# Kernel tuning notes

Hardware: AMD Instinct MI355X
Metric: run time of the kernel (lower is better)

The kernel has to match this reference:

```python
import jax, jax.numpy as jnp
import numpy as np

HEADS = 16
DIM_HEAD = 64
LN_EPS = 1e-5


def setup_inputs() -> dict:
    key = jax.random.key(0)
    ks = jax.random.split(key, 4)
    b, n, dim = 2, 2048, 1024
    inner = HEADS * DIM_HEAD
    x = jax.random.normal(ks[0], (b, n, dim), dtype=jnp.float32)
    gamma = jnp.ones((dim,), dtype=jnp.float32)
    beta = jnp.zeros((dim,), dtype=jnp.float32)
    w_qkv = jax.random.normal(ks[1], (dim, 3 * inner), dtype=jnp.float32) * (dim ** -0.5)
    w_out = jax.random.normal(ks[2], (inner, dim), dtype=jnp.float32) * (inner ** -0.5)
    b_out = jnp.zeros((dim,), dtype=jnp.float32)
    return {"x": x, "gamma": gamma, "beta": beta, "w_qkv": w_qkv, "w_out": w_out, "b_out": b_out}


def reference(x, gamma, beta, w_qkv, w_out, b_out):
    b, n, dim = x.shape
    h, d = HEADS, DIM_HEAD
    scale = d ** -0.5
    # LayerNorm
    mu = jnp.mean(x, axis=-1, keepdims=True)
    var = jnp.mean(jnp.square(x - mu), axis=-1, keepdims=True)
    xn = (x - mu) * jax.lax.rsqrt(var + LN_EPS) * gamma + beta
    # QKV projection (no bias)
    qkv = xn @ w_qkv  # [b, n, 3*h*d]
    q, k, v = jnp.split(qkv, 3, axis=-1)
    split_heads = lambda t: t.reshape(b, n, h, d).transpose(0, 2, 1, 3)  # [b, h, n, d]
    q, k, v = split_heads(q), split_heads(k), split_heads(v)
    q = q * scale
    sim = jnp.einsum('bhid,bhjd->bhij', q, k)  # full O(n^2) score matrix
    attn = jax.nn.softmax(sim, axis=-1)
    out = jnp.einsum('bhij,bhjd->bhid', attn, v)
    out = out.transpose(0, 2, 1, 3).reshape(b, n, h * d)
    return out @ w_out + b_out
```

## Files before the change

kernel.cpp:

```cpp
#include <hip/hip_runtime.h>
#include <hip/hip_bf16.h>

#define HEADS 16
#define DH 64
#define DIM 1024
#define SEQ 2048
#define BATCH 2
#define ROWS (BATCH*SEQ)
#define NQKV (3*DIM)
#define NKVT (SEQ/64)
#define NSPLIT 2
#define QSCALE 0.18033688011112042f
#define NBH (BATCH*HEADS)
#define NQROWS (NBH*SEQ)

typedef __attribute__((ext_vector_type(8))) short bf16x8;
typedef __attribute__((ext_vector_type(4))) float f32x4;
typedef __attribute__((ext_vector_type(16))) float f32x16;
typedef __attribute__((ext_vector_type(4))) unsigned u32x4;
typedef __hip_bfloat16 bf16;

static __device__ __forceinline__ bf16 f2bf(float v){ return __float2bfloat16(v); }

static __device__ __forceinline__ unsigned cvtpk(float a, float b){
  unsigned r;
  asm("v_cvt_pk_bf16_f32 %0, %1, %2" : "=v"(r) : "v"(a), "v"(b));
  return r;
}

static __device__ __forceinline__ void gload16(const void* g, void* lds){
  __builtin_amdgcn_global_load_lds((const __attribute__((address_space(1))) void*)g,
                                   (__attribute__((address_space(3))) void*)lds, 16, 0, 0);
}

__global__ __launch_bounds__(256) void prep_kernel(
    const float* __restrict__ x, const float* __restrict__ gamma,
    const float* __restrict__ beta, bf16* __restrict__ xn,
    const float* __restrict__ w_qkv, bf16* __restrict__ wqt,
    const float* __restrict__ w_out, bf16* __restrict__ wot)
{
  __shared__ float red[8];
  __shared__ __align__(16) bf16 tt[64][72];
  int bid = blockIdx.x;
  int tid = threadIdx.x;
  if (bid < ROWS){
    int row = bid;
    float4 v = ((const float4*)(x + (size_t)row*DIM))[tid];
    float s  = v.x+v.y+v.z+v.w;
    float ss = v.x*v.x+v.y*v.y+v.z*v.z+v.w*v.w;
    #pragma unroll
    for (int m=1;m<64;m<<=1){ s += __shfl_xor(s,m); ss += __shfl_xor(ss,m); }
    int wid = tid>>6;
    if ((tid&63)==0){ red[wid]=s; red[4+wid]=ss; }
    __syncthreads();
    s  = red[0]+red[1]+red[2]+red[3];
    ss = red[4]+red[5]+red[6]+red[7];
    float mu  = s*(1.0f/DIM);
    float var = ss*(1.0f/DIM) - mu*mu;
    float inv = rsqrtf(var + 1e-5f);
    float4 g  = ((const float4*)gamma)[tid];
    float4 bb = ((const float4*)beta)[tid];
    __align__(8) bf16 o[4];
    o[0]=f2bf((v.x-mu)*inv*g.x+bb.x);
    o[1]=f2bf((v.y-mu)*inv*g.y+bb.y);
    o[2]=f2bf((v.z-mu)*inv*g.z+bb.z);
    o[3]=f2bf((v.w-mu)*inv*g.w+bb.w);
    *(uint2*)&xn[(size_t)row*DIM + tid*4] = *(const uint2*)o;
    return;
  }
  const float* in; bf16* out; int R, C, bx, by;
  if (bid < ROWS + 768){
    int idx = bid - ROWS; bx = idx % 48; by = idx / 48;
    in = w_qkv; out = wqt; R = DIM; C = NQKV;
  } else {
    int idx = bid - ROWS - 768; bx = idx % 16; by = idx / 16;
    in = w_out; out = wot; R = DIM; C = DIM;
  }
  int c0 = bx*64, r0 = by*64;
  int row = tid>>2;
  int cq  = (tid&3)*16;
  #pragma unroll
  for (int j=0;j<4;j++){
    float4 v = *(const float4*)&in[(size_t)(r0+row)*C + c0 + cq + j*4];
    tt[cq+j*4+0][row] = f2bf(v.x);
    tt[cq+j*4+1][row] = f2bf(v.y);
    tt[cq+j*4+2][row] = f2bf(v.z);
    tt[cq+j*4+3][row] = f2bf(v.w);
  }
  __syncthreads();
  int c = tid>>2; int rq = (tid&3)*16;
  uint4 u0 = *(const uint4*)&tt[c][rq];
  uint4 u1 = *(const uint4*)&tt[c][rq+8];
  *(uint4*)&out[(size_t)(c0+c)*R + r0 + rq]     = u0;
  *(uint4*)&out[(size_t)(c0+c)*R + r0 + rq + 8] = u1;
}

template<int BM>
__global__ __launch_bounds__(256) void gemm_bt(
    const bf16* __restrict__ A, const bf16* __restrict__ Bt, int K, int mode,
    bf16* __restrict__ qb, bf16* __restrict__ kb, bf16* __restrict__ vtb,
    float* __restrict__ outf, const float* __restrict__ bias)
{
  constexpr int MT = (BM == 128) ? 4 : 2;
  constexpr int NT = (BM == 128) ? 4 : 2;
  __shared__ __align__(16) bf16 aL[3][BM*32];
  __shared__ __align__(16) bf16 bL[3][BM*32];
  int tid = threadIdx.x;
  int w = tid>>6, l = tid&63;
  int lr = l&15, lh = l>>4;
  int wr = w>>1, wc = w&1;
  int nbx = gridDim.x;
  int lin = blockIdx.y*nbx + blockIdx.x;
  int cpx = (nbx*gridDim.y) >> 3;
  int nl  = (lin & 7)*cpx + (lin >> 3);
  int bx = nl % nbx, by = nl / nbx;
  const bf16* Ab = A  + (size_t)(by*BM)*K;
  const bf16* Bb = Bt + (size_t)(bx*BM)*K;
  int srow = w*32 + (l>>2);
  int scol = ((l&3)*8) ^ (((l>>2)&3)<<3);
  int frsw = (lr&3)<<3;
  int nt = K/32;

  f32x4 acc[MT][NT] = {};

  auto STAGE = [&](int buf, int k0){
    if constexpr (BM == 128){
      gload16(Ab + (size_t)(srow   )*K + k0 + scol, &aL[buf][w*1024      ]);
      gload16(Ab + (size_t)(srow+16)*K + k0 + scol, &aL[buf][w*1024 + 512]);
      gload16(Bb + (size_t)(srow   )*K + k0 + scol, &bL[buf][w*1024      ]);
      gload16(Bb + (size_t)(srow+16)*K + k0 + scol, &bL[buf][w*1024 + 512]);
    } else {
      gload16(Ab + (size_t)(tid>>2)*K + k0 + scol, &aL[buf][w*512]);
      gload16(Bb + (size_t)(tid>>2)*K + k0 + scol, &bL[buf][w*512]);
    }
  };

  auto COMPUTE = [&](int buf){
    bf16x8 af[MT], bfr[NT];
    #pragma unroll
    for (int m=0;m<MT;m++)
      af[m]  = *(const bf16x8*)&aL[buf][(wr*(MT*16) + m*16 + lr)*32 + ((lh*8) ^ frsw)];
    #pragma unroll
    for (int n=0;n<NT;n++)
      bfr[n] = *(const bf16x8*)&bL[buf][(wc*(NT*16) + n*16 + lr)*32 + ((lh*8) ^ frsw)];
    #pragma unroll
    for (int m=0;m<MT;m++)
      #pragma unroll
      for (int n=0;n<NT;n++)
        acc[m][n] = __builtin_amdgcn_mfma_f32_16x16x32_bf16(af[m], bfr[n], acc[m][n], 0,0,0);
  };

  STAGE(0, 0);
  STAGE(1, 32);
  int cur = 0;
  for (int t=0; t<nt-1; t++){
    if constexpr (BM == 128) asm volatile("s_waitcnt vmcnt(4)" ::: "memory");
    else                     asm volatile("s_waitcnt vmcnt(2)" ::: "memory");
    __builtin_amdgcn_s_barrier();
    __builtin_amdgcn_sched_barrier(0);
    int s2 = cur + 2; if (s2 >= 3) s2 -= 3;
    if (t+2 < nt) STAGE(s2, (t+2)*32);
    COMPUTE(cur);
    cur = (cur == 2) ? 0 : cur + 1;
  }
  asm volatile("s_waitcnt vmcnt(0)" ::: "memory");
  __builtin_amdgcn_s_barrier();
  __builtin_amdgcn_sched_barrier(0);
  COMPUTE(cur);

  int rb = by*BM + wr*(MT*16), cb = bx*BM + wc*(NT*16);
  if (mode == 1){
    #pragma unroll
    for (int m=0;m<MT;m++)
      #pragma unroll
      for (int n=0;n<NT;n++)
        #pragma unroll
        for (int reg=0;reg<4;reg++){
          int r = rb + m*16 + lh*4 + reg;
          int c = cb + n*16 + lr;
          outf[(size_t)r*DIM + c] = acc[m][n][reg] + bias[c];
        }
  } else if (bx < 8){
    int b = rb >> 11;
    int nn0 = rb & 2047;
    #pragma unroll
    for (int m=0;m<MT;m++)
      #pragma unroll
      for (int n=0;n<NT;n++)
        #pragma unroll
        for (int reg=0;reg<4;reg++){
          int nn = nn0 + m*16 + lh*4 + reg;
          int c  = cb + n*16 + lr;
          int hh = c >> 6, dd = c & 63;
          qb[((size_t)(b*HEADS + hh)*SEQ + nn)*DH + dd] = f2bf(acc[m][n][reg]*QSCALE);
        }
  } else if (bx < 16){
    int b = rb >> 11;
    int kvt = (rb & 2047) >> 6;
    int hh0 = ((cb - 1024) >> 6);
    #pragma unroll
    for (int m=0;m<MT;m++)
      #pragma unroll
      for (int reg=0;reg<4;reg++){
        int kvi = m*16 + lh*4 + reg;
        int sw  = (kvi&7)<<3;
        #pragma unroll
        for (int n=0;n<NT;n++){
          int dd = n*16 + lr;
          kb[((size_t)(b*HEADS + hh0)*NKVT + kvt)*4096 + kvi*64 + (dd ^ sw)] = f2bf(acc[m][n][reg]);
        }
      }
  } else {
    __syncthreads();
    bf16* tl = (w < 2 ? (bf16*)aL : (bf16*)bL) + (w&1)*4096;
    int b   = rb >> 11;
    int kvt = (rb & 2047) >> 6;
    int hh  = (cb - 2048) >> 6;
    #pragma unroll
    for (int n=0;n<NT;n++){
      int dd = n*16 + lr;
      int sw = (dd&7)<<3;
      #pragma unroll
      for (int m=0;m<MT;m++)
        #pragma unroll
        for (int reg=0;reg<4;reg++)
          tl[dd*64 + ((m*16 + lh*4 + reg) ^ sw)] = f2bf(acc[m][n][reg]);
    }
    __syncthreads();
    size_t gb = ((size_t)(b*HEADS + hh)*NKVT + kvt)*4096;
    #pragma unroll
    for (int j=0;j<8;j++)
      *(uint4*)&vtb[gb + j*512 + l*8] = *(const uint4*)&tl[j*512 + l*8];
  }
}

__global__ __launch_bounds__(256,4) void attn_part(
    const bf16* __restrict__ qb, const bf16* __restrict__ kb,
    const bf16* __restrict__ vtb,
    bf16* __restrict__ Opart, float* __restrict__ Mpart, float* __restrict__ Spart)
{
  __shared__ __align__(16) bf16 Kl[2][4096];
  __shared__ __align__(16) bf16 Vl[2][4096];
  int tid = threadIdx.x;
  int w = tid>>6, l = tid&63;
  int q5 = l & 31;
  int hi = l >> 5;
  int swz = (q5&7)<<3;
  int lin = (blockIdx.z*gridDim.y + blockIdx.y)*gridDim.x + blockIdx.x;
  int nl  = (lin & 7)*128 + (lin >> 3);
  int bqx = nl & 15;
  int bh  = (nl >> 4) & 31;
  int sp  = nl >> 9;
  int ts = sp*16, te = ts+16;
  const bf16* Q  = qb  + (size_t)bh*SEQ*DH;
  const bf16* Kt = kb  + (size_t)bh*NKVT*4096;
  const bf16* Vt = vtb + (size_t)bh*NKVT*4096;
  int q0w = bqx*128 + w*32;

  int co[4];
  #pragma unroll
  for (int st=0;st<4;st++) co[st] = (st*16 + hi*8) ^ swz;
  int r0 = q5*64, r1 = r0 + 2048;

  bf16x8 qf[4];
  #pragma unroll
  for (int st=0;st<4;st++)
    qf[st] = *(const bf16x8*)&Q[(size_t)(q0w + q5)*DH + st*16 + hi*8];

  bf16x8 vone;
  #pragma unroll
  for (int i=0;i<8;i++) vone[i] = (short)0x3f80;

  f32x16 o0 = {}, o1 = {}, osum = {};
  float mrun = -3e38f;

  {
    const bf16* ks = Kt + (size_t)ts*4096;
    const bf16* vs = Vt + (size_t)ts*4096;
    gload16(ks + w*1024       + l*8, &Kl[0][w*1024      ]);
    gload16(ks + w*1024 + 512 + l*8, &Kl[0][w*1024 + 512]);
    gload16(vs + w*1024       + l*8, &Vl[0][w*1024      ]);
    gload16(vs + w*1024 + 512 + l*8, &Vl[0][w*1024 + 512]);
  }

  for (int t=ts; t<te; t++){
    int cur = (t-ts)&1;
    __syncthreads();
    if (t+1 < te){
      const bf16* ks = Kt + (size_t)(t+1)*4096;
      const bf16* vs = Vt + (size_t)(t+1)*4096;
      gload16(ks + w*1024       + l*8, &Kl[cur^1][w*1024      ]);
      gload16(ks + w*1024 + 512 + l*8, &Kl[cur^1][w*1024 + 512]);
      gload16(vs + w*1024       + l*8, &Vl[cur^1][w*1024      ]);
      gload16(vs + w*1024 + 512 + l*8, &Vl[cur^1][w*1024 + 512]);
    }
    f32x16 s0 = {}, s1 = {};
    __builtin_amdgcn_s_setprio(1);
    #pragma unroll
    for (int st=0;st<4;st++){
      bf16x8 kf0 = *(const bf16x8*)&Kl[cur][r0 + co[st]];
      bf16x8 kf1 = *(const bf16x8*)&Kl[cur][r1 + co[st]];
      s0 = __builtin_amdgcn_mfma_f32_32x32x16_bf16(kf0, qf[st], s0, 0,0,0);
      s1 = __builtin_amdgcn_mfma_f32_32x32x16_bf16(kf1, qf[st], s1, 0,0,0);
    }
    __builtin_amdgcn_s_setprio(0);
    float pm = -3e38f;
    #pragma unroll
    for (int r=0;r<16;r++) pm = fmaxf(fmaxf(pm, s0[r]), s1[r]);
    pm = fmaxf(pm, __shfl_xor(pm, 32));
    if (__any(pm > mrun + 8.f)){
      float mn = fmaxf(mrun, pm);
      float sc = __builtin_amdgcn_exp2f(mrun - mn);
      mrun = mn;
      #pragma unroll
      for (int reg=0;reg<16;reg++){
        float scr = __shfl(sc, (l & 32) | ((reg&3) + 8*(reg>>2) + 4*hi));
        o0[reg] *= scr;
        o1[reg] *= scr;
        osum[reg] *= scr;
      }
    }
    #pragma unroll
    for (int r=0;r<16;r++){
      s0[r] = __builtin_amdgcn_exp2f(s0[r] - mrun);
      s1[r] = __builtin_amdgcn_exp2f(s1[r] - mrun);
    }
    #define PV_STEP(SV, SGN, KVS)                                                    \
    {                                                                                \
      unsigned Aw = cvtpk(SV[SGN+0], SV[SGN+1]);                                     \
      unsigned Bw = cvtpk(SV[SGN+2], SV[SGN+3]);                                     \
      unsigned Cw = cvtpk(SV[SGN+4], SV[SGN+5]);                                     \
      unsigned Dw = cvtpk(SV[SGN+6], SV[SGN+7]);                                     \
      asm volatile("v_permlane32_swap_b32 %0, %1" : "+v"(Aw), "+v"(Cw));             \
      asm volatile("v_permlane32_swap_b32 %0, %1" : "+v"(Bw), "+v"(Dw));             \
      u32x4 pw = {Aw, Bw, Cw, Dw};                                                   \
      bf16x8 pa = *(const bf16x8*)&pw;                                               \
      bf16x8 vf0 = *(const bf16x8*)&Vl[cur][r0 + co[KVS]];                           \
      bf16x8 vf1 = *(const bf16x8*)&Vl[cur][r1 + co[KVS]];                           \
      __builtin_amdgcn_s_setprio(1);                                                 \
      o0 = __builtin_amdgcn_mfma_f32_32x32x16_bf16(pa, vf0, o0, 0,0,0);              \
      o1 = __builtin_amdgcn_mfma_f32_32x32x16_bf16(pa, vf1, o1, 0,0,0);              \
      osum = __builtin_amdgcn_mfma_f32_32x32x16_bf16(pa, vone, osum, 0,0,0);         \
      __builtin_amdgcn_s_setprio(0);                                                 \
    }
    PV_STEP(s0, 0, 0)
    PV_STEP(s0, 8, 1)
    PV_STEP(s1, 0, 2)
    PV_STEP(s1, 8, 3)
    #undef PV_STEP
  }
  size_t rbase = ((size_t)sp*NBH + bh)*SEQ;
  #pragma unroll
  for (int reg=0;reg<16;reg++){
    int q = q0w + (reg&3) + 8*(reg>>2) + 4*hi;
    Opart[(rbase + q)*64 + q5]      = f2bf(o0[reg]);
    Opart[(rbase + q)*64 + 32 + q5] = f2bf(o1[reg]);
  }
  if (l < 32)
    Mpart[rbase + q0w + l] = mrun;
  if (q5 == 0){
    #pragma unroll
    for (int reg=0;reg<16;reg++){
      int q = q0w + (reg&3) + 8*(reg>>2) + 4*hi;
      Spart[rbase + q] = osum[reg];
    }
  }
}

__global__ __launch_bounds__(256) void attn_merge(
    const bf16* __restrict__ Opart, const float* __restrict__ Mpart,
    const float* __restrict__ Spart, bf16* __restrict__ ao)
{
  int r = blockIdx.x*4 + (threadIdx.x>>6);
  int d = threadIdx.x & 63;
  float m0 = Mpart[r], m1 = Mpart[NQROWS + r];
  float m  = fmaxf(m0, m1);
  float c0 = exp2f(m0 - m), c1 = exp2f(m1 - m);
  float denom = Spart[r]*c0 + Spart[NQROWS + r]*c1;
  float v = __bfloat162float(Opart[(size_t)r*64 + d])*c0
          + __bfloat162float(Opart[((size_t)NQROWS + r)*64 + d])*c1;
  int bh = r >> 11, q = r & 2047;
  int b = bh >> 4, h = bh & 15;
  ao[((size_t)(b*SEQ + q))*DIM + h*DH + d] = f2bf(v / denom);
}

extern "C" void kernel_launch(void* const* d_in, const int* in_sizes, int n_in,
                              void* d_out, int out_size, void* d_ws, size_t ws_size,
                              hipStream_t stream)
{
  const float* x     = (const float*)d_in[0];
  const float* gamma = (const float*)d_in[1];
  const float* beta  = (const float*)d_in[2];
  const float* w_qkv = (const float*)d_in[3];
  const float* w_out = (const float*)d_in[4];
  const float* b_out = (const float*)d_in[5];
  float* out = (float*)d_out;

  bf16* ws  = (bf16*)d_ws;
  bf16* xn  = ws;
  bf16* wqt = xn  + (size_t)ROWS*DIM;
  bf16* wot = wqt + (size_t)NQKV*DIM;
  bf16* qb  = wot + (size_t)DIM*DIM;
  bf16* kb  = qb  + (size_t)NBH*SEQ*DH;
  bf16* vtb = kb  + (size_t)NBH*SEQ*DH;
  bf16* ao  = vtb + (size_t)NBH*SEQ*DH;
  bf16* Opart = ao + (size_t)ROWS*DIM;
  float* Mpart = (float*)(Opart + (size_t)NSPLIT*NQROWS*DH);
  float* Spart = Mpart + (size_t)NSPLIT*NQROWS;

  prep_kernel<<<dim3(ROWS + 768 + 256), dim3(256), 0, stream>>>(
      x, gamma, beta, xn, w_qkv, wqt, w_out, wot);
  gemm_bt<128><<<dim3(NQKV/128, ROWS/128), dim3(256), 0, stream>>>(
      xn, wqt, DIM, 0, qb, kb, vtb, (float*)nullptr, (const float*)nullptr);
  attn_part<<<dim3(SEQ/128, NBH, NSPLIT), dim3(256), 0, stream>>>(
      qb, kb, vtb, Opart, Mpart, Spart);
  attn_merge<<<dim3(NQROWS/4), dim3(256), 0, stream>>>(Opart, Mpart, Spart, ao);
  gemm_bt<64><<<dim3(DIM/64, ROWS/64), dim3(256), 0, stream>>>(
      ao, wot, DIM, 1, (bf16*)nullptr, (bf16*)nullptr, (bf16*)nullptr, out, b_out);
}
```

Baseline: 122.8 us.

## Fuse split-KV merge into attention kernel via last-arriver atomic flag

Removes the separate attn_merge launch. Each attention block bumps an atomic counter per (head, query tile) once its partial output is written, and the second block to finish merges both partials and writes the bf16 attention output directly. The flags are zeroed by an extra block in the prep kernel. This saves a kernel launch and a grid-wide dependency, but adds threadfences, an atomic per block, and a serial merge tail inside some attention blocks.

```diff
diff --git a/kernel.cpp b/kernel.cpp
--- a/kernel.cpp
+++ b/kernel.cpp
@@ -13,6 +13,7 @@
 #define QSCALE 0.18033688011112042f
 #define NBH (BATCH*HEADS)
 #define NQROWS (NBH*SEQ)
+#define NFLAGS 512
 
 typedef __attribute__((ext_vector_type(8))) short bf16x8;
 typedef __attribute__((ext_vector_type(4))) float f32x4;
@@ -37,12 +38,18 @@
     const float* __restrict__ x, const float* __restrict__ gamma,
     const float* __restrict__ beta, bf16* __restrict__ xn,
     const float* __restrict__ w_qkv, bf16* __restrict__ wqt,
-    const float* __restrict__ w_out, bf16* __restrict__ wot)
+    const float* __restrict__ w_out, bf16* __restrict__ wot,
+    int* __restrict__ flags)
 {
   __shared__ float red[8];
   __shared__ __align__(16) bf16 tt[64][72];
   int bid = blockIdx.x;
   int tid = threadIdx.x;
+  if (bid == ROWS + 768 + 256){
+    flags[tid] = 0;
+    flags[tid + 256] = 0;
+    return;
+  }
   if (bid < ROWS){
     int row = bid;
     float4 v = ((const float4*)(x + (size_t)row*DIM))[tid];
@@ -237,10 +244,12 @@
 __global__ __launch_bounds__(256,4) void attn_part(
     const bf16* __restrict__ qb, const bf16* __restrict__ kb,
     const bf16* __restrict__ vtb,
-    bf16* __restrict__ Opart, float* __restrict__ Mpart, float* __restrict__ Spart)
+    bf16* __restrict__ Opart, float* __restrict__ Mpart, float* __restrict__ Spart,
+    int* __restrict__ flags, bf16* __restrict__ ao)
 {
   __shared__ __align__(16) bf16 Kl[2][4096];
   __shared__ __align__(16) bf16 Vl[2][4096];
+  __shared__ int oldf;
   int tid = threadIdx.x;
   int w = tid>>6, l = tid&63;
   int q5 = l & 31;
@@ -365,23 +374,42 @@
       Spart[rbase + q] = osum[reg];
     }
   }
-}
-
-__global__ __launch_bounds__(256) void attn_merge(
-    const bf16* __restrict__ Opart, const float* __restrict__ Mpart,
-    const float* __restrict__ Spart, bf16* __restrict__ ao)
-{
-  int r = blockIdx.x*4 + (threadIdx.x>>6);
-  int d = threadIdx.x & 63;
-  float m0 = Mpart[r], m1 = Mpart[NQROWS + r];
-  float m  = fmaxf(m0, m1);
-  float c0 = exp2f(m0 - m), c1 = exp2f(m1 - m);
-  float denom = Spart[r]*c0 + Spart[NQROWS + r]*c1;
-  float v = __bfloat162float(Opart[(size_t)r*64 + d])*c0
-          + __bfloat162float(Opart[((size_t)NQROWS + r)*64 + d])*c1;
-  int bh = r >> 11, q = r & 2047;
-  int b = bh >> 4, h = bh & 15;
-  ao[((size_t)(b*SEQ + q))*DIM + h*DH + d] = f2bf(v / denom);
+
+  __threadfence();
+  if (tid == 0) oldf = atomicAdd(&flags[bh*16 + bqx], 1);
+  __syncthreads();
+  if (oldf == 1){
+    __threadfence();
+    int rrow = tid >> 3;
+    int d0   = (tid & 7) * 8;
+    int b = bh >> 4, h = bh & 15;
+    #pragma unroll
+    for (int it=0; it<4; it++){
+      int q = bqx*128 + it*32 + rrow;
+      size_t r = (size_t)bh*SEQ + q;
+      float m0 = Mpart[r], m1 = Mpart[NQROWS + r];
+      float S0 = Spart[r], S1 = Spart[NQROWS + r];
+      float mm = fmaxf(m0, m1);
+      float c0 = exp2f(m0 - mm), c1 = exp2f(m1 - mm);
+      float inv = 1.f / (S0*c0 + S1*c1);
+      c0 *= inv; c1 *= inv;
+      uint4 u0 = *(const uint4*)&Opart[r*64 + d0];
+      uint4 u1 = *(const uint4*)&Opart[((size_t)NQROWS + r)*64 + d0];
+      unsigned res[4];
+      unsigned ua[4] = {u0.x, u0.y, u0.z, u0.w};
+      unsigned ub[4] = {u1.x, u1.y, u1.z, u1.w};
+      #pragma unroll
+      for (int j=0;j<4;j++){
+        float a_lo = __uint_as_float(ua[j] << 16);
+        float a_hi = __uint_as_float(ua[j] & 0xffff0000u);
+        float b_lo = __uint_as_float(ub[j] << 16);
+        float b_hi = __uint_as_float(ub[j] & 0xffff0000u);
+        res[j] = cvtpk(a_lo*c0 + b_lo*c1, a_hi*c0 + b_hi*c1);
+      }
+      uint4 rv = {res[0], res[1], res[2], res[3]};
+      *(uint4*)&ao[((size_t)(b*SEQ + q))*DIM + h*DH + d0] = rv;
+    }
+  }
 }
 
 extern "C" void kernel_launch(void* const* d_in, const int* in_sizes, int n_in,
@@ -407,14 +435,14 @@
   bf16* Opart = ao + (size_t)ROWS*DIM;
   float* Mpart = (float*)(Opart + (size_t)NSPLIT*NQROWS*DH);
   float* Spart = Mpart + (size_t)NSPLIT*NQROWS;
-
-  prep_kernel<<<dim3(ROWS + 768 + 256), dim3(256), 0, stream>>>(
-      x, gamma, beta, xn, w_qkv, wqt, w_out, wot);
+  int*   flags = (int*)(Spart + (size_t)NSPLIT*NQROWS);
+
+  prep_kernel<<<dim3(ROWS + 768 + 256 + 1), dim3(256), 0, stream>>>(
+      x, gamma, beta, xn, w_qkv, wqt, w_out, wot, flags);
   gemm_bt<128><<<dim3(NQKV/128, ROWS/128), dim3(256), 0, stream>>>(
       xn, wqt, DIM, 0, qb, kb, vtb, (float*)nullptr, (const float*)nullptr);
   attn_part<<<dim3(SEQ/128, NBH, NSPLIT), dim3(256), 0, stream>>>(
-      qb, kb, vtb, Opart, Mpart, Spart);
-  attn_merge<<<dim3(NQROWS/4), dim3(256), 0, stream>>>(Opart, Mpart, Spart, ao);
+      qb, kb, vtb, Opart, Mpart, Spart, flags, ao);
   gemm_bt<64><<<dim3(DIM/64, ROWS/64), dim3(256), 0, stream>>>(
       ao, wot, DIM, 1, (bf16*)nullptr, (bf16*)nullptr, (bf16*)nullptr, out, b_out);
 }
```

Measured after the change: 303.7 us. 147% more time.
